# Kernel tuning notes

Hardware: AMD Instinct MI355X
Metric: run time of the kernel (lower is better)

## Reference

```python
import jax, jax.numpy as jnp
import numpy as np

B, S, E, H = 2, 2048, 1024, 16
D = E // H  # head_dim = 64


def setup_inputs() -> dict:
    key = jax.random.key(0)
    ks = jax.random.split(key, 9)
    sc = 1.0 / np.sqrt(E)
    return {
        "x": jax.random.normal(ks[0], (B, S, E), dtype=jnp.float32),
        "Wq": jax.random.normal(ks[1], (E, E), dtype=jnp.float32) * sc,
        "bq": jnp.zeros((E,), dtype=jnp.float32),
        "Wk": jax.random.normal(ks[2], (E, E), dtype=jnp.float32) * sc,
        "bk": jnp.zeros((E,), dtype=jnp.float32),
        "Wv": jax.random.normal(ks[3], (E, E), dtype=jnp.float32) * sc,
        "bv": jnp.zeros((E,), dtype=jnp.float32),
        "Wo": jax.random.normal(ks[4], (E, E), dtype=jnp.float32) * sc,
        "bo": jnp.zeros((E,), dtype=jnp.float32),
    }


def reference(x, Wq, bq, Wk, bk, Wv, bv, Wo, bo):
    b, s, e = x.shape
    # projections: [B,S,E] -> [B,H,S,D]
    def heads(w, bias):
        return (x @ w + bias).reshape(b, s, H, D).transpose(0, 2, 1, 3)
    q, k, v = heads(Wq, bq), heads(Wk, bk), heads(Wv, bv)
    # scores [B,H,S,S]
    scores = jnp.einsum("bhqd,bhkd->bhqk", q, k) / jnp.sqrt(jnp.float32(D))
    causal = jnp.tril(jnp.ones((s, s), dtype=bool))
    scores = jnp.where(causal[None, None], scores, -jnp.inf)
    weights = jax.nn.softmax(scores, axis=-1)
    out = jnp.einsum("bhqk,bhkd->bhqd", weights, v)
    out = out.transpose(0, 2, 1, 3).reshape(b, s, e)
    return out @ Wo + bo
```

## Files before the change

### kernel.cpp

```cpp
#include <hip/hip_runtime.h>
#include <hip/hip_bf16.h>

#define B_SZ 2
#define S_LEN 2048
#define E_DIM 1024
#define NH 16
#define DH 64
#define M_ROWS (B_SZ * S_LEN)
#define QB 128
#define KVB 64

typedef __attribute__((ext_vector_type(8))) short short8;
typedef __attribute__((ext_vector_type(4))) float floatx4;
typedef __attribute__((ext_vector_type(4))) int intx4;

static __device__ __forceinline__ unsigned short f2bf(float f) {
    __hip_bfloat16 h = __float2bfloat16(f);
    return *reinterpret_cast<unsigned short*>(&h);
}
static __device__ __forceinline__ float bf2f(unsigned short u) {
    unsigned int v = ((unsigned int)u) << 16;
    return __builtin_bit_cast(float, v);
}
static __device__ __forceinline__ unsigned int pack2bf(float lo, float hi) {
    return (unsigned int)f2bf(lo) | ((unsigned int)f2bf(hi) << 16);
}

static __device__ __forceinline__ void gl2lds16(const void* g, void* l) {
    __builtin_amdgcn_global_load_lds((const __attribute__((address_space(1))) void*)g,
                                     (__attribute__((address_space(3))) void*)l, 16, 0, 0);
}

#define WAIT_VM0() asm volatile("s_waitcnt vmcnt(0)" ::: "memory")
#define WAIT_LGKM0() asm volatile("s_waitcnt lgkmcnt(0)" ::: "memory")

__global__ __launch_bounds__(256) void prep(const float* __restrict__ x,
                                            unsigned short* __restrict__ Xb,
                                            const float* __restrict__ W0,
                                            const float* __restrict__ W1,
                                            const float* __restrict__ W2,
                                            const float* __restrict__ W3,
                                            unsigned short* __restrict__ T0,
                                            unsigned short* __restrict__ T1,
                                            unsigned short* __restrict__ T2,
                                            unsigned short* __restrict__ T3) {
    __shared__ float tile[32][33];
    int bid = blockIdx.x;
    int t = threadIdx.x;
    if (bid < 4096) {
        int i = (bid * 256 + t) * 4;
        float4 v = *reinterpret_cast<const float4*>(x + i);
        ushort4 o;
        o.x = f2bf(v.x); o.y = f2bf(v.y); o.z = f2bf(v.z); o.w = f2bf(v.w);
        *reinterpret_cast<ushort4*>(Xb + i) = o;
        return;
    }
    int u = bid - 4096;
    int z = u >> 10, rest = u & 1023;
    int bx = (rest & 31) * 32, by = (rest >> 5) * 32;
    const float* W = (z == 0) ? W0 : (z == 1) ? W1 : (z == 2) ? W2 : W3;
    unsigned short* Wt = (z == 0) ? T0 : (z == 1) ? T1 : (z == 2) ? T2 : T3;
    int tx = t & 31, ty = t >> 5;
#pragma unroll
    for (int i = 0; i < 32; i += 8)
        tile[ty + i][tx] = W[(size_t)(by + ty + i) * E_DIM + bx + tx];
    __syncthreads();
#pragma unroll
    for (int i = 0; i < 32; i += 8)
        Wt[(size_t)(bx + ty + i) * E_DIM + by + tx] = f2bf(tile[tx][ty + i]);
}

#define QSCALE 0.18033688011112042f

__global__ __launch_bounds__(512, 2) void gemm_qkv8(const unsigned short* __restrict__ Wcat,
                                                    const unsigned short* __restrict__ Xb,
                                                    const float* __restrict__ bq,
                                                    const float* __restrict__ bk,
                                                    const float* __restrict__ bv,
                                                    unsigned short* __restrict__ Qg,
                                                    unsigned short* __restrict__ Kg,
                                                    unsigned short* __restrict__ Vtg) {
    __shared__ __align__(16) char lds[2][2][32768];

    int t = threadIdx.x;
    int b = blockIdx.x;
    int xcd = b & 7, ii = b >> 3;
    int it = (xcd & 3) * 3 + (ii >> 3);
    int jt = (xcd >> 2) * 8 + (ii & 7);
    int iBase = it << 8, jBase = jt << 8;

    int w = t >> 6, lane = t & 63;
    int lr = lane & 15, lh = lane >> 4;
    int wm = w >> 2, wn = w & 3;

    int srow = t >> 3;
    int scbx = ((t & 7) << 4) ^ ((srow & 7) << 4);

    const char* Ab = (const char*)Wcat;
    const char* Bb = (const char*)Xb;

    floatx4 acc[8][4];
#pragma unroll
    for (int i = 0; i < 8; i++)
#pragma unroll
        for (int j = 0; j < 4; j++) acc[i][j] = (floatx4){0.f, 0.f, 0.f, 0.f};

    auto stageA = [&](int buf, int kt) {
        int k0b = kt << 7;
#pragma unroll
        for (int c = 0; c < 4; c++)
            gl2lds16(Ab + (size_t)(iBase + c * 64 + srow) * 2048 + k0b + scbx,
                     &lds[buf][0][c * 8192 + t * 16]);
    };
    auto stageB = [&](int buf, int kt) {
        int k0b = kt << 7;
#pragma unroll
        for (int c = 0; c < 4; c++)
            gl2lds16(Bb + (size_t)(jBase + c * 64 + srow) * 2048 + k0b + scbx,
                     &lds[buf][1][c * 8192 + t * 16]);
    };

    short8 af[4][2], bf[4][2];
    auto rdA = [&](int buf, int qm) {
#pragma unroll
        for (int mi = 0; mi < 4; mi++)
#pragma unroll
            for (int ks = 0; ks < 2; ks++) {
                int row = wm * 128 + qm * 64 + mi * 16 + lr;
                af[mi][ks] = *reinterpret_cast<const short8*>(
                    &lds[buf][0][(row * 128 + ks * 64 + lh * 16) ^ ((row & 7) << 4)]);
            }
    };
    auto rdB = [&](int buf, int qn) {
#pragma unroll
        for (int ni = 0; ni < 2; ni++)
#pragma unroll
            for (int ks = 0; ks < 2; ks++) {
                int row = wn * 64 + qn * 32 + ni * 16 + lr;
                bf[qn * 2 + ni][ks] = *reinterpret_cast<const short8*>(
                    &lds[buf][1][(row * 128 + ks * 64 + lh * 16) ^ ((row & 7) << 4)]);
            }
    };
    auto mfma16 = [&](int qm, int qn) {
        __builtin_amdgcn_s_setprio(1);
#pragma unroll
        for (int mi = 0; mi < 4; mi++)
#pragma unroll
            for (int ni = 0; ni < 2; ni++)
#pragma unroll
                for (int ks = 0; ks < 2; ks++)
                    acc[qm * 4 + mi][qn * 2 + ni] = __builtin_amdgcn_mfma_f32_16x16x32_bf16(
                        af[mi][ks], bf[qn * 2 + ni][ks], acc[qm * 4 + mi][qn * 2 + ni], 0, 0, 0);
        __builtin_amdgcn_s_setprio(0);
    };

    const int NT = 16;
    stageA(0, 0);
    stageB(0, 0);
    WAIT_VM0();
    __builtin_amdgcn_s_barrier();

    for (int kt = 0; kt < NT; ++kt) {
        int cur = kt & 1, nxt = cur ^ 1;
        bool pf = (kt + 1 < NT);
        rdA(cur, 0);
        rdB(cur, 0);
        if (pf) stageA(nxt, kt + 1);
        __builtin_amdgcn_s_barrier();
        WAIT_LGKM0();
        __builtin_amdgcn_sched_barrier(0);
        mfma16(0, 0);
        __builtin_amdgcn_s_barrier();
        rdB(cur, 1);
        if (pf) stageB(nxt, kt + 1);
        __builtin_amdgcn_s_barrier();
        WAIT_LGKM0();
        __builtin_amdgcn_sched_barrier(0);
        mfma16(0, 1);
        __builtin_amdgcn_s_barrier();
        rdA(cur, 1);
        __builtin_amdgcn_s_barrier();
        WAIT_LGKM0();
        __builtin_amdgcn_sched_barrier(0);
        mfma16(1, 0);
        __builtin_amdgcn_s_barrier();
        if (pf) WAIT_VM0();
        __builtin_amdgcn_s_barrier();
        mfma16(1, 1);
        __builtin_amdgcn_s_barrier();
    }

    int wsel = iBase >> 10;
    const float* bias = (wsel == 0) ? bq : (wsel == 1) ? bk : bv;
    __syncthreads();

    if (wsel < 2) {
        unsigned short* O = wsel ? Kg : Qg;
        float scale = wsel ? 1.0f : QSCALE;
#pragma unroll
        for (int mi8 = 0; mi8 < 8; mi8++) {
            int i = iBase + wm * 128 + mi8 * 16 + lh * 4;
            int im = i & 1023;
            int h = im >> 6, d0 = im & 63;
            float4 bs = *reinterpret_cast<const float4*>(&bias[im]);
#pragma unroll
            for (int nf = 0; nf < 4; nf++) {
                int j = jBase + wn * 64 + nf * 16 + lr;
                int b_ = j >> 11, s = j & (S_LEN - 1);
                ushort4 pk;
                pk.x = f2bf((acc[mi8][nf][0] + bs.x) * scale);
                pk.y = f2bf((acc[mi8][nf][1] + bs.y) * scale);
                pk.z = f2bf((acc[mi8][nf][2] + bs.z) * scale);
                pk.w = f2bf((acc[mi8][nf][3] + bs.w) * scale);
                *reinterpret_cast<ushort4*>(
                    &O[((size_t)(b_ * NH + h) * S_LEN + s) * DH + d0]) = pk;
            }
        }
    } else {
        char* lw = &lds[0][0][0] + w * 16384;
#pragma unroll
        for (int mi8 = 0; mi8 < 8; mi8++) {
            int i = iBase + wm * 128 + mi8 * 16 + lh * 4;
            float4 bs = *reinterpret_cast<const float4*>(&bias[i & 1023]);
#pragma unroll
            for (int nf = 0; nf < 4; nf++) {
                int jl = nf * 16 + lr;
#pragma unroll
                for (int r = 0; r < 4; r++) {
                    int il = mi8 * 16 + lh * 4 + r;
                    float bb = (r == 0) ? bs.x : (r == 1) ? bs.y : (r == 2) ? bs.z : bs.w;
                    *reinterpret_cast<unsigned short*>(
                        lw + ((il * 128 + jl * 2) ^ ((il & 7) << 4))) =
                        f2bf(acc[mi8][nf][r] + bb);
                }
            }
        }
        __syncthreads();
#pragma unroll
        for (int rep = 0; rep < 16; rep++) {
            int idx = rep * 64 + lane;
            int il = idx >> 3, jb = idx & 7;
            short8 vv = *reinterpret_cast<const short8*>(
                lw + ((il * 128 + jb * 16) ^ ((il & 7) << 4)));
            int i = iBase + wm * 128 + il;
            int im = i & 1023;
            int h = im >> 6, d = im & 63;
            int j = jBase + wn * 64 + jb * 8;
            int b_ = j >> 11, s = j & (S_LEN - 1);
            *reinterpret_cast<short8*>(
                &Vtg[((size_t)(b_ * NH + h) * DH + d) * S_LEN + s]) = vv;
        }
    }
}

__global__ __launch_bounds__(512, 2) void gemm_o8(const unsigned short* __restrict__ Wot,
                                                  const unsigned short* __restrict__ Og,
                                                  const float* __restrict__ bo,
                                                  float* __restrict__ out) {
    __shared__ __align__(16) char lds[2][2][16384];

    int t = threadIdx.x;
    int b = blockIdx.x;
    int xcd = b & 7, ii = b >> 3;
    int it = ii & 7;
    int jt = (xcd << 2) | (ii >> 3);
    int iBase = it << 7, jBase = jt << 7;

    int w = t >> 6, lane = t & 63;
    int lr = lane & 15, lh = lane >> 4;
    int wm = w >> 2, wn = w & 3;

    int srow = t >> 3;
    int scbx = ((t & 7) << 4) ^ ((srow & 7) << 4);

    const char* Ab = (const char*)Wot;
    const char* Bb = (const char*)Og;

    floatx4 acc[4][2];
#pragma unroll
    for (int i = 0; i < 4; i++)
#pragma unroll
        for (int j = 0; j < 2; j++) acc[i][j] = (floatx4){0.f, 0.f, 0.f, 0.f};

    auto stageA = [&](int buf, int kt) {
        int k0b = kt << 7;
#pragma unroll
        for (int c = 0; c < 2; c++)
            gl2lds16(Ab + (size_t)(iBase + c * 64 + srow) * 2048 + k0b + scbx,
                     &lds[buf][0][c * 8192 + t * 16]);
    };
    auto stageB = [&](int buf, int kt) {
        int k0b = kt << 7;
#pragma unroll
        for (int c = 0; c < 2; c++)
            gl2lds16(Bb + (size_t)(jBase + c * 64 + srow) * 2048 + k0b + scbx,
                     &lds[buf][1][c * 8192 + t * 16]);
    };

    short8 af[4][2], bf[2][2];
    auto rdA = [&](int buf, int qm) {
#pragma unroll
        for (int m2 = 0; m2 < 2; m2++)
#pragma unroll
            for (int ks = 0; ks < 2; ks++) {
                int mi = qm * 2 + m2;
                int row = wm * 64 + mi * 16 + lr;
                af[mi][ks] = *reinterpret_cast<const short8*>(
                    &lds[buf][0][(row * 128 + ks * 64 + lh * 16) ^ ((row & 7) << 4)]);
            }
    };
    auto rdB = [&](int buf) {
#pragma unroll
        for (int nf = 0; nf < 2; nf++)
#pragma unroll
            for (int ks = 0; ks < 2; ks++) {
                int row = wn * 32 + nf * 16 + lr;
                bf[nf][ks] = *reinterpret_cast<const short8*>(
                    &lds[buf][1][(row * 128 + ks * 64 + lh * 16) ^ ((row & 7) << 4)]);
            }
    };
    auto mfma8 = [&](int qm) {
        __builtin_amdgcn_s_setprio(1);
#pragma unroll
        for (int m2 = 0; m2 < 2; m2++)
#pragma unroll
            for (int nf = 0; nf < 2; nf++)
#pragma unroll
                for (int ks = 0; ks < 2; ks++) {
                    int mi = qm * 2 + m2;
                    acc[mi][nf] = __builtin_amdgcn_mfma_f32_16x16x32_bf16(
                        af[mi][ks], bf[nf][ks], acc[mi][nf], 0, 0, 0);
                }
        __builtin_amdgcn_s_setprio(0);
    };

    const int NT = 16;
    stageA(0, 0);
    stageB(0, 0);
    WAIT_VM0();
    __builtin_amdgcn_s_barrier();

    for (int kt = 0; kt < NT; ++kt) {
        int cur = kt & 1, nxt = cur ^ 1;
        bool pf = (kt + 1 < NT);
        rdA(cur, 0);
        rdB(cur);
        if (pf) stageA(nxt, kt + 1);
        __builtin_amdgcn_s_barrier();
        WAIT_LGKM0();
        __builtin_amdgcn_sched_barrier(0);
        mfma8(0);
        __builtin_amdgcn_s_barrier();
        rdA(cur, 1);
        if (pf) stageB(nxt, kt + 1);
        __builtin_amdgcn_s_barrier();
        WAIT_LGKM0();
        __builtin_amdgcn_sched_barrier(0);
        mfma8(1);
        if (pf) WAIT_VM0();
        __builtin_amdgcn_s_barrier();
    }

#pragma unroll
    for (int mi = 0; mi < 4; mi++) {
        int i = iBase + wm * 64 + mi * 16 + lh * 4;
        float4 bs = *reinterpret_cast<const float4*>(&bo[i]);
#pragma unroll
        for (int nf = 0; nf < 2; nf++) {
            int j = jBase + wn * 32 + nf * 16 + lr;
            float4 o;
            o.x = acc[mi][nf][0] + bs.x;
            o.y = acc[mi][nf][1] + bs.y;
            o.z = acc[mi][nf][2] + bs.z;
            o.w = acc[mi][nf][3] + bs.w;
            *reinterpret_cast<float4*>(&out[(size_t)j * E_DIM + i]) = o;
        }
    }
}

__global__ __launch_bounds__(256, 4) void attn_fwd(const unsigned short* __restrict__ Qg,
                                                   const unsigned short* __restrict__ Kg,
                                                   const unsigned short* __restrict__ Vtg,
                                                   unsigned short* __restrict__ Og,
                                                   unsigned short* __restrict__ Opart,
                                                   float* __restrict__ lpart) {
    __shared__ __align__(16) char kt_lds[2][KVB * 128];
    __shared__ __align__(16) char vt_lds[2][KVB * 128];

    int bid = blockIdx.x;
    int xcd = bid & 7, ii = bid >> 3;
    int bh = (xcd << 2) + ii / 30;
    int jj = 29 - (ii % 30);
    int qb, ch, c;
    if (jj < 6)        { qb = jj; ch = 0; c = 1; }
    else if (jj < 18)  { int u = jj - 6;  qb = 6 + (u >> 1); ch = u & 1; c = 2; }
    else               { int u = jj - 18; qb = 12 + u / 3;   ch = u % 3; c = 3; }
    int T = 2 * qb + 2;
    int kt_lo = ch * T / c;
    int kt_hi = (ch + 1) * T / c - 1;
    bool split = (c > 1);

    int w = threadIdx.x >> 6, lane = threadIdx.x & 63;
    int lr = lane & 15, lh = lane >> 4;
    int q0 = qb * QB + w * 32;

    const char* Kb = (const char*)(Kg + (size_t)bh * S_LEN * DH);
    const char* Vb = (const char*)(Vtg + (size_t)bh * DH * S_LEN);
    const unsigned short* Qb = Qg + (size_t)bh * S_LEN * DH;

    int wi0 = w * 2;
    int srow0 = wi0 * 8 + (lane >> 3);
    int scol = (lane & 7) << 4;

    auto stage = [&](int buf, int kt) {
        int kv0 = kt * KVB;
#pragma unroll
        for (int i = 0; i < 2; ++i) {
            int row = srow0 + i * 8;
            int colb = scol ^ ((row & 7) << 4);
            gl2lds16(Kb + (size_t)(kv0 + row) * 128 + colb,
                     kt_lds[buf] + (wi0 + i) * 1024);
            gl2lds16(Vb + (size_t)row * (S_LEN * 2) + (size_t)kv0 * 2 + colb,
                     vt_lds[buf] + (wi0 + i) * 1024);
        }
    };

    short8 aq[2][2];
#pragma unroll
    for (int m = 0; m < 2; m++)
#pragma unroll
        for (int ks = 0; ks < 2; ks++)
            aq[m][ks] = *reinterpret_cast<const short8*>(
                Qb + (size_t)(q0 + m * 16 + lr) * DH + ks * 32 + lh * 8);

    floatx4 oacc[2][4];
    float lsum[2];
#pragma unroll
    for (int m = 0; m < 2; m++) {
#pragma unroll
        for (int dt = 0; dt < 4; dt++) oacc[m][dt] = (floatx4){0.f, 0.f, 0.f, 0.f};
        lsum[m] = 0.f;
    }

    stage(0, kt_lo);
    __syncthreads();
    int buf = 0;

    for (int kt = kt_lo; kt <= kt_hi; ++kt) {
        if (kt < kt_hi) stage(buf ^ 1, kt + 1);
        int kv0 = kt * KVB;
        bool skip = (kv0 > q0 + 31);
        if (!skip) {
            const char* Kt = kt_lds[buf];
            const char* Vt = vt_lds[buf];
            floatx4 sacc[2][4];
#pragma unroll
            for (int m = 0; m < 2; m++)
#pragma unroll
                for (int nt = 0; nt < 4; nt++) sacc[m][nt] = (floatx4){0.f, 0.f, 0.f, 0.f};
#pragma unroll
            for (int ks = 0; ks < 2; ks++)
#pragma unroll
                for (int nt = 0; nt < 4; nt++) {
                    int row = nt * 16 + lr;
                    int addr = (row * 128 + ks * 64 + lh * 16) ^ ((row & 7) << 4);
                    short8 bk = *reinterpret_cast<const short8*>(Kt + addr);
#pragma unroll
                    for (int m = 0; m < 2; m++)
                        sacc[m][nt] = __builtin_amdgcn_mfma_f32_16x16x32_bf16(
                            bk, aq[m][ks], sacc[m][nt], 0, 0, 0);
                }
            if (kv0 + KVB - 1 > q0) {
#pragma unroll
                for (int m = 0; m < 2; m++)
#pragma unroll
                    for (int nt = 0; nt < 4; nt++)
#pragma unroll
                        for (int r = 0; r < 4; r++) {
                            int kcol = kv0 + nt * 16 + lh * 4 + r;
                            int qrow = q0 + m * 16 + lr;
                            if (kcol > qrow) sacc[m][nt][r] = -1e30f;
                        }
            }
            unsigned int pk[2][4][2];
#pragma unroll
            for (int m = 0; m < 2; m++) {
                float ls = 0.f;
#pragma unroll
                for (int nt = 0; nt < 4; nt++) {
#pragma unroll
                    for (int r = 0; r < 4; r++) {
                        float p = __builtin_amdgcn_exp2f(sacc[m][nt][r]);
                        sacc[m][nt][r] = p;
                        ls += p;
                    }
                    pk[m][nt][0] = pack2bf(sacc[m][nt][0], sacc[m][nt][1]);
                    pk[m][nt][1] = pack2bf(sacc[m][nt][2], sacc[m][nt][3]);
                }
                lsum[m] += ls;
            }
            short8 pa[2][2];
            int hsel = lh >> 1;
#pragma unroll
            for (int m = 0; m < 2; m++)
#pragma unroll
                for (int ks = 0; ks < 2; ks++) {
                    intx4 u;
#pragma unroll
                    for (int t4 = 0; t4 < 4; t4++) {
                        int src = lr + 32 * (lh & 1) + 16 * (t4 >> 1);
                        int r0 = __shfl((int)pk[m][2 * ks][t4 & 1], src);
                        int r1 = __shfl((int)pk[m][2 * ks + 1][t4 & 1], src);
                        u[t4] = hsel ? r1 : r0;
                    }
                    pa[m][ks] = __builtin_bit_cast(short8, u);
                }
#pragma unroll
            for (int ks = 0; ks < 2; ks++)
#pragma unroll
                for (int dt = 0; dt < 4; dt++) {
                    int row = dt * 16 + lr;
                    int addr = (row * 128 + ks * 64 + lh * 16) ^ ((row & 7) << 4);
                    short8 bv = *reinterpret_cast<const short8*>(Vt + addr);
#pragma unroll
                    for (int m = 0; m < 2; m++)
                        oacc[m][dt] = __builtin_amdgcn_mfma_f32_16x16x32_bf16(
                            pa[m][ks], bv, oacc[m][dt], 0, 0, 0);
                }
        }
        __syncthreads();
        buf ^= 1;
    }

#pragma unroll
    for (int m = 0; m < 2; m++) {
        lsum[m] += __shfl_xor(lsum[m], 16);
        lsum[m] += __shfl_xor(lsum[m], 32);
    }

    if (split) {
        int base = (qb < 12) ? (qb - 6) * 2 : 12 + (qb - 12) * 3;
        int pi = bh * 24 + base + ch;
        unsigned short* Op = Opart + (size_t)pi * (QB * DH);
        float* lp = lpart + (size_t)pi * QB;
#pragma unroll
        for (int m = 0; m < 2; m++) {
            if (lh == 0) lp[w * 32 + m * 16 + lr] = lsum[m];
#pragma unroll
            for (int r = 0; r < 4; r++) {
                int row = w * 32 + m * 16 + lh * 4 + r;
#pragma unroll
                for (int dt = 0; dt < 4; dt++)
                    Op[row * DH + dt * 16 + lr] = f2bf(oacc[m][dt][r]);
            }
        }
    } else {
        int b_ = bh >> 4, h_ = bh & 15;
#pragma unroll
        for (int m = 0; m < 2; m++) {
#pragma unroll
            for (int r = 0; r < 4; r++) {
                float lv = __shfl(lsum[m], lh * 4 + r);
                float inv = 1.f / lv;
                int srow = q0 + m * 16 + lh * 4 + r;
#pragma unroll
                for (int dt = 0; dt < 4; dt++)
                    Og[((size_t)b_ * S_LEN + srow) * E_DIM + h_ * 64 + dt * 16 + lr] =
                        f2bf(oacc[m][dt][r] * inv);
            }
        }
    }
}

__global__ __launch_bounds__(256) void attn_reduce(const unsigned short* __restrict__ Opart,
                                                   const float* __restrict__ lpart,
                                                   unsigned short* __restrict__ Og) {
    int bh = blockIdx.x;
    int qb = 6 + blockIdx.y;
    int c = (qb < 12) ? 2 : 3;
    int base = (qb < 12) ? (qb - 6) * 2 : 12 + (qb - 12) * 3;
    int pi0 = bh * 24 + base;
    const unsigned short* P0 = Opart + (size_t)pi0 * (QB * DH);
    const float* l0 = lpart + (size_t)pi0 * QB;
    int t = threadIdx.x;
    int cg = t & 7, r0 = t >> 3;
    int b_ = bh >> 4, h_ = bh & 15;
    int qrow0 = qb * QB;
#pragma unroll
    for (int rr = 0; rr < 4; rr++) {
        int row = r0 + rr * 32;
        float ls = l0[row] + l0[QB + row];
        if (c == 3) ls += l0[2 * QB + row];
        float inv = 1.f / ls;
        short8 v0 = *reinterpret_cast<const short8*>(P0 + row * DH + cg * 8);
        short8 v1 = *reinterpret_cast<const short8*>(P0 + QB * DH + row * DH + cg * 8);
        float s[8];
#pragma unroll
        for (int j = 0; j < 8; j++)
            s[j] = bf2f((unsigned short)v0[j]) + bf2f((unsigned short)v1[j]);
        if (c == 3) {
            short8 v2 = *reinterpret_cast<const short8*>(P0 + 2 * QB * DH + row * DH + cg * 8);
#pragma unroll
            for (int j = 0; j < 8; j++) s[j] += bf2f((unsigned short)v2[j]);
        }
        short8 o;
#pragma unroll
        for (int j = 0; j < 8; j++) o[j] = (short)f2bf(s[j] * inv);
        *reinterpret_cast<short8*>(Og + ((size_t)b_ * S_LEN + qrow0 + row) * E_DIM +
                                   h_ * 64 + cg * 8) = o;
    }
}

extern "C" void kernel_launch(void* const* d_in, const int* in_sizes, int n_in,
                              void* d_out, int out_size, void* d_ws, size_t ws_size,
                              hipStream_t stream) {
    const float* x  = (const float*)d_in[0];
    const float* Wq = (const float*)d_in[1];
    const float* bq = (const float*)d_in[2];
    const float* Wk = (const float*)d_in[3];
    const float* bk = (const float*)d_in[4];
    const float* Wv = (const float*)d_in[5];
    const float* bv = (const float*)d_in[6];
    const float* Wo = (const float*)d_in[7];
    const float* bo = (const float*)d_in[8];
    float* out = (float*)d_out;

    const size_t NX = (size_t)M_ROWS * E_DIM;
    const size_t NW = (size_t)E_DIM * E_DIM;
    unsigned short* ws  = (unsigned short*)d_ws;
    unsigned short* Xb  = ws;
    unsigned short* Wqt = Xb + NX;
    unsigned short* Wkt = Wqt + NW;
    unsigned short* Wvt = Wkt + NW;
    unsigned short* Wot = Wvt + NW;
    unsigned short* Qg  = Wot + NW;
    unsigned short* Kg  = Qg + NX;
    unsigned short* Vtg = Kg + NX;
    unsigned short* Og  = Vtg + NX;
    unsigned short* Opart = Xb;
    float* lpart = (float*)(Opart + (size_t)32 * 24 * QB * DH);

    prep<<<dim3(8192), 256, 0, stream>>>(x, Xb, Wq, Wk, Wv, Wo, Wqt, Wkt, Wvt, Wot);

    gemm_qkv8<<<dim3(192), 512, 0, stream>>>(Wqt, Xb, bq, bk, bv, Qg, Kg, Vtg);

    attn_fwd<<<dim3(960), 256, 0, stream>>>(Qg, Kg, Vtg, Og, Opart, lpart);
    attn_reduce<<<dim3(B_SZ * NH, 10), 256, 0, stream>>>(Opart, lpart, Og);

    gemm_o8<<<dim3(256), 512, 0, stream>>>(Wot, Og, bo, out);
}
```

Baseline: 113.9 us.

## Retile QKV GEMM to 192x256 tiles so 256 blocks fill all CUs

The fused QKV projection GEMM drops its output tile from 256x256 to 192x256, so the grid grows from 192 to 256 workgroups and matches the CU count, reducing idle CUs. The epilogue is rewritten to work per 16-row fragment, because one tile can now straddle the Q/K/V boundary. The V transpose now goes through a small per-wave padded LDS buffer instead of a full-tile staging area. In exchange, each block gets less operand reuse per tile, and the launch bound drops to one block per CU.

```diff
diff --git a/kernel.cpp b/kernel.cpp
--- a/kernel.cpp
+++ b/kernel.cpp
@@ -72,7 +72,7 @@
 
 #define QSCALE 0.18033688011112042f
 
-__global__ __launch_bounds__(512, 2) void gemm_qkv8(const unsigned short* __restrict__ Wcat,
+__global__ __launch_bounds__(512, 1) void gemm_qkv8(const unsigned short* __restrict__ Wcat,
                                                     const unsigned short* __restrict__ Xb,
                                                     const float* __restrict__ bq,
                                                     const float* __restrict__ bk,
@@ -80,14 +80,14 @@
                                                     unsigned short* __restrict__ Qg,
                                                     unsigned short* __restrict__ Kg,
                                                     unsigned short* __restrict__ Vtg) {
-    __shared__ __align__(16) char lds[2][2][32768];
+    __shared__ __align__(16) char lds[2][57344];
 
     int t = threadIdx.x;
     int b = blockIdx.x;
     int xcd = b & 7, ii = b >> 3;
-    int it = (xcd & 3) * 3 + (ii >> 3);
+    int it = (xcd & 3) * 4 + (ii >> 3);
     int jt = (xcd >> 2) * 8 + (ii & 7);
-    int iBase = it << 8, jBase = jt << 8;
+    int iBase = it * 192, jBase = jt << 8;
 
     int w = t >> 6, lane = t & 63;
     int lr = lane & 15, lh = lane >> 4;
@@ -99,58 +99,58 @@
     const char* Ab = (const char*)Wcat;
     const char* Bb = (const char*)Xb;
 
-    floatx4 acc[8][4];
-#pragma unroll
-    for (int i = 0; i < 8; i++)
+    floatx4 acc[6][4];
+#pragma unroll
+    for (int i = 0; i < 6; i++)
 #pragma unroll
         for (int j = 0; j < 4; j++) acc[i][j] = (floatx4){0.f, 0.f, 0.f, 0.f};
 
     auto stageA = [&](int buf, int kt) {
         int k0b = kt << 7;
 #pragma unroll
-        for (int c = 0; c < 4; c++)
+        for (int c = 0; c < 3; c++)
             gl2lds16(Ab + (size_t)(iBase + c * 64 + srow) * 2048 + k0b + scbx,
-                     &lds[buf][0][c * 8192 + t * 16]);
+                     &lds[buf][c * 8192 + t * 16]);
     };
     auto stageB = [&](int buf, int kt) {
         int k0b = kt << 7;
 #pragma unroll
         for (int c = 0; c < 4; c++)
             gl2lds16(Bb + (size_t)(jBase + c * 64 + srow) * 2048 + k0b + scbx,
-                     &lds[buf][1][c * 8192 + t * 16]);
-    };
-
-    short8 af[4][2], bf[4][2];
+                     &lds[buf][24576 + c * 8192 + t * 16]);
+    };
+
+    short8 af[3][2], bf[4][2];
     auto rdA = [&](int buf, int qm) {
 #pragma unroll
-        for (int mi = 0; mi < 4; mi++)
+        for (int ml = 0; ml < 3; ml++)
 #pragma unroll
             for (int ks = 0; ks < 2; ks++) {
-                int row = wm * 128 + qm * 64 + mi * 16 + lr;
-                af[mi][ks] = *reinterpret_cast<const short8*>(
-                    &lds[buf][0][(row * 128 + ks * 64 + lh * 16) ^ ((row & 7) << 4)]);
+                int row = wm * 96 + (qm * 3 + ml) * 16 + lr;
+                af[ml][ks] = *reinterpret_cast<const short8*>(
+                    &lds[buf][(row * 128 + ks * 64 + lh * 16) ^ ((row & 7) << 4)]);
             }
     };
     auto rdB = [&](int buf, int qn) {
 #pragma unroll
-        for (int ni = 0; ni < 2; ni++)
+        for (int nl = 0; nl < 2; nl++)
 #pragma unroll
             for (int ks = 0; ks < 2; ks++) {
-                int row = wn * 64 + qn * 32 + ni * 16 + lr;
-                bf[qn * 2 + ni][ks] = *reinterpret_cast<const short8*>(
-                    &lds[buf][1][(row * 128 + ks * 64 + lh * 16) ^ ((row & 7) << 4)]);
-            }
-    };
-    auto mfma16 = [&](int qm, int qn) {
+                int row = wn * 64 + (qn * 2 + nl) * 16 + lr;
+                bf[qn * 2 + nl][ks] = *reinterpret_cast<const short8*>(
+                    &lds[buf][24576 + ((row * 128 + ks * 64 + lh * 16) ^ ((row & 7) << 4))]);
+            }
+    };
+    auto mfma12 = [&](int qm, int qn) {
         __builtin_amdgcn_s_setprio(1);
 #pragma unroll
-        for (int mi = 0; mi < 4; mi++)
-#pragma unroll
-            for (int ni = 0; ni < 2; ni++)
+        for (int ml = 0; ml < 3; ml++)
+#pragma unroll
+            for (int nl = 0; nl < 2; nl++)
 #pragma unroll
                 for (int ks = 0; ks < 2; ks++)
-                    acc[qm * 4 + mi][qn * 2 + ni] = __builtin_amdgcn_mfma_f32_16x16x32_bf16(
-                        af[mi][ks], bf[qn * 2 + ni][ks], acc[qm * 4 + mi][qn * 2 + ni], 0, 0, 0);
+                    acc[qm * 3 + ml][qn * 2 + nl] = __builtin_amdgcn_mfma_f32_16x16x32_bf16(
+                        af[ml][ks], bf[qn * 2 + nl][ks], acc[qm * 3 + ml][qn * 2 + nl], 0, 0, 0);
         __builtin_amdgcn_s_setprio(0);
     };
 
@@ -169,86 +169,76 @@
         __builtin_amdgcn_s_barrier();
         WAIT_LGKM0();
         __builtin_amdgcn_sched_barrier(0);
-        mfma16(0, 0);
+        mfma12(0, 0);
         __builtin_amdgcn_s_barrier();
         rdB(cur, 1);
         if (pf) stageB(nxt, kt + 1);
         __builtin_amdgcn_s_barrier();
         WAIT_LGKM0();
         __builtin_amdgcn_sched_barrier(0);
-        mfma16(0, 1);
+        mfma12(0, 1);
         __builtin_amdgcn_s_barrier();
         rdA(cur, 1);
         __builtin_amdgcn_s_barrier();
         WAIT_LGKM0();
         __builtin_amdgcn_sched_barrier(0);
-        mfma16(1, 0);
+        mfma12(1, 0);
         __builtin_amdgcn_s_barrier();
         if (pf) WAIT_VM0();
         __builtin_amdgcn_s_barrier();
-        mfma16(1, 1);
-        __builtin_amdgcn_s_barrier();
-    }
-
-    int wsel = iBase >> 10;
-    const float* bias = (wsel == 0) ? bq : (wsel == 1) ? bk : bv;
+        mfma12(1, 1);
+        __builtin_amdgcn_s_barrier();
+    }
+
     __syncthreads();
-
-    if (wsel < 2) {
-        unsigned short* O = wsel ? Kg : Qg;
-        float scale = wsel ? 1.0f : QSCALE;
-#pragma unroll
-        for (int mi8 = 0; mi8 < 8; mi8++) {
-            int i = iBase + wm * 128 + mi8 * 16 + lh * 4;
-            int im = i & 1023;
-            int h = im >> 6, d0 = im & 63;
-            float4 bs = *reinterpret_cast<const float4*>(&bias[im]);
+    unsigned short* vt = reinterpret_cast<unsigned short*>(&lds[0][0] + w * 2560);
+
+#pragma unroll
+    for (int mi = 0; mi < 6; mi++) {
+        int i0 = iBase + wm * 96 + mi * 16;
+        int wsel = i0 >> 10;
+        int im = i0 & 1023;
+        const float* bias = (wsel == 0) ? bq : (wsel == 1) ? bk : bv;
+        float4 bs = *reinterpret_cast<const float4*>(&bias[im + lh * 4]);
+        if (wsel < 2) {
+            unsigned short* O = wsel ? Kg : Qg;
+            float scale = wsel ? 1.0f : QSCALE;
+            int h = im >> 6, d0 = (im & 63) + lh * 4;
 #pragma unroll
             for (int nf = 0; nf < 4; nf++) {
                 int j = jBase + wn * 64 + nf * 16 + lr;
                 int b_ = j >> 11, s = j & (S_LEN - 1);
                 ushort4 pk;
-                pk.x = f2bf((acc[mi8][nf][0] + bs.x) * scale);
-                pk.y = f2bf((acc[mi8][nf][1] + bs.y) * scale);
-                pk.z = f2bf((acc[mi8][nf][2] + bs.z) * scale);
-                pk.w = f2bf((acc[mi8][nf][3] + bs.w) * scale);
+                pk.x = f2bf((acc[mi][nf][0] + bs.x) * scale);
+                pk.y = f2bf((acc[mi][nf][1] + bs.y) * scale);
+                pk.z = f2bf((acc[mi][nf][2] + bs.z) * scale);
+                pk.w = f2bf((acc[mi][nf][3] + bs.w) * scale);
                 *reinterpret_cast<ushort4*>(
                     &O[((size_t)(b_ * NH + h) * S_LEN + s) * DH + d0]) = pk;
             }
-        }
-    } else {
-        char* lw = &lds[0][0][0] + w * 16384;
-#pragma unroll
-        for (int mi8 = 0; mi8 < 8; mi8++) {
-            int i = iBase + wm * 128 + mi8 * 16 + lh * 4;
-            float4 bs = *reinterpret_cast<const float4*>(&bias[i & 1023]);
-#pragma unroll
-            for (int nf = 0; nf < 4; nf++) {
-                int jl = nf * 16 + lr;
+        } else {
+#pragma unroll
+            for (int nf = 0; nf < 4; nf++)
 #pragma unroll
                 for (int r = 0; r < 4; r++) {
-                    int il = mi8 * 16 + lh * 4 + r;
                     float bb = (r == 0) ? bs.x : (r == 1) ? bs.y : (r == 2) ? bs.z : bs.w;
-                    *reinterpret_cast<unsigned short*>(
-                        lw + ((il * 128 + jl * 2) ^ ((il & 7) << 4))) =
-                        f2bf(acc[mi8][nf][r] + bb);
+                    vt[(lh * 4 + r) * 80 + nf * 16 + lr] = f2bf(acc[mi][nf][r] + bb);
                 }
-            }
-        }
-        __syncthreads();
-#pragma unroll
-        for (int rep = 0; rep < 16; rep++) {
-            int idx = rep * 64 + lane;
-            int il = idx >> 3, jb = idx & 7;
-            short8 vv = *reinterpret_cast<const short8*>(
-                lw + ((il * 128 + jb * 16) ^ ((il & 7) << 4)));
-            int i = iBase + wm * 128 + il;
-            int im = i & 1023;
-            int h = im >> 6, d = im & 63;
-            int j = jBase + wn * 64 + jb * 8;
-            int b_ = j >> 11, s = j & (S_LEN - 1);
-            *reinterpret_cast<short8*>(
-                &Vtg[((size_t)(b_ * NH + h) * DH + d) * S_LEN + s]) = vv;
+            WAIT_LGKM0();
+            __builtin_amdgcn_sched_barrier(0);
+            int h = im >> 6, d0 = im & 63;
+#pragma unroll
+            for (int p = 0; p < 2; p++) {
+                int idx = p * 64 + lane;
+                int dl = idx >> 3, sg = idx & 7;
+                short8 vv = *reinterpret_cast<const short8*>(&vt[dl * 80 + sg * 8]);
+                int j = jBase + wn * 64 + sg * 8;
+                int b_ = j >> 11, s = j & (S_LEN - 1);
+                *reinterpret_cast<short8*>(
+                    &Vtg[((size_t)(b_ * NH + h) * DH + d0 + dl) * S_LEN + s]) = vv;
+            }
+            WAIT_LGKM0();
+            __builtin_amdgcn_sched_barrier(0);
         }
     }
 }
@@ -642,7 +632,7 @@
 
     prep<<<dim3(8192), 256, 0, stream>>>(x, Xb, Wq, Wk, Wv, Wo, Wqt, Wkt, Wvt, Wot);
 
-    gemm_qkv8<<<dim3(192), 512, 0, stream>>>(Wqt, Xb, bq, bk, bv, Qg, Kg, Vtg);
+    gemm_qkv8<<<dim3(256), 512, 0, stream>>>(Wqt, Xb, bq, bk, bv, Qg, Kg, Vtg);
 
     attn_fwd<<<dim3(960), 256, 0, stream>>>(Qg, Kg, Vtg, Og, Opart, lpart);
     attn_reduce<<<dim3(B_SZ * NH, 10), 256, 0, stream>>>(Opart, lpart, Og);
```

New measurement: 107.1 us. 1.06x faster.
